# Kernel tuning notes

Hardware: AMD Instinct MI355X
Metric: run time of the kernel (lower is better)

## Reference

```python
import jax, jax.numpy as jnp
import numpy as np

N_NODES = 100000
N_EDGES = 3200000
IN_DIM = 512
HIDDEN = 16
N_CLASSES = 7


def setup_inputs() -> dict:
    key = jax.random.key(0)
    k1, k2, k3, k4 = jax.random.split(key, 4)
    x = jax.random.normal(k1, (N_NODES, IN_DIM), dtype=jnp.float32)
    edge_index = jax.random.randint(k2, (2, N_EDGES), 0, N_NODES, dtype=jnp.int32)
    W1 = jax.random.normal(k3, (IN_DIM, HIDDEN), dtype=jnp.float32) / np.sqrt(IN_DIM)
    b1 = jnp.zeros((HIDDEN,), dtype=jnp.float32)
    W2 = jax.random.normal(k4, (HIDDEN, N_CLASSES), dtype=jnp.float32) / np.sqrt(HIDDEN)
    b2 = jnp.zeros((N_CLASSES,), dtype=jnp.float32)
    return {"x": x, "edge_index": edge_index, "W1": W1, "b1": b1, "W2": W2, "b2": b2}


def _gcn_norm(edge_index, num_nodes):
    # Add self loops and compute symmetric normalization D^{-1/2} A D^{-1/2}
    loop = jnp.arange(num_nodes, dtype=edge_index.dtype)
    src = jnp.concatenate([edge_index[0], loop])
    dst = jnp.concatenate([edge_index[1], loop])
    deg = jax.ops.segment_sum(jnp.ones_like(dst, dtype=jnp.float32), dst,
                              num_segments=num_nodes)
    dinv = jnp.where(deg > 0, jax.lax.rsqrt(deg), 0.0)
    norm = dinv[src] * dinv[dst]  # [E + N]
    return src, dst, norm


def _gcn_conv(x, W, b, src, dst, norm, num_nodes):
    h = x @ W                                   # [N, out] dense GEMM first (PyG order)
    msg = h[src] * norm[:, None]                # gather + per-edge scale
    agg = jax.ops.segment_sum(msg, dst, num_segments=num_nodes)  # scatter-add
    return agg + b


def reference(x, edge_index, W1, b1, W2, b2):
    n = x.shape[0]
    src, dst, norm = _gcn_norm(edge_index, n)
    h = _gcn_conv(x, W1, b1, src, dst, norm, n)
    h = jax.nn.relu(h)
    # dropout is identity in eval mode (deterministic reference)
    out = _gcn_conv(h, W2, b2, src, dst, norm, n)
    return jax.nn.log_softmax(out, axis=1)
```

## Files before the change

### kernel.cpp

```cpp
#include <hip/hip_runtime.h>

#define N_NODES 100000
#define N_EDGES 3200000
#define IN_DIM  512
#define HIDDEN  16
#define NCLS    7

#define BSH     9
#define BNODES  512
#define NB      ((N_NODES + BNODES - 1) / BNODES)

#define EPB1    8192
#define NBLK1   ((N_EDGES + EPB1 - 1) / EPB1)
#define EPB2    4096
#define NBLK2   ((N_EDGES + EPB2 - 1) / EPB2)

__global__ void k_zero(int* __restrict__ bcnt, int* __restrict__ rowstart) {
    int i = threadIdx.x;
    bcnt[i] = 0;
    if (i == 0) rowstart[N_NODES] = N_EDGES;
}

__global__ __launch_bounds__(256) void k_bcount(const int* __restrict__ dst,
                                                int* __restrict__ bcnt) {
    __shared__ int hist[256];
    int tid = threadIdx.x;
    hist[tid] = 0;
    __syncthreads();
    int e0 = blockIdx.x * EPB1;
    int n  = min(EPB1, N_EDGES - e0);
    for (int k = tid; k < n; k += 256)
        atomicAdd(&hist[dst[e0 + k] >> BSH], 1);
    __syncthreads();
    int c = hist[tid];
    if (c) atomicAdd(&bcnt[tid], c);
}

__global__ __launch_bounds__(256) void k_bscan(const int* __restrict__ bcnt,
                                               int* __restrict__ bstart,
                                               int* __restrict__ bcur) {
    __shared__ int s[256];
    int tid = threadIdx.x;
    int c = bcnt[tid];
    s[tid] = c;
    __syncthreads();
    for (int off = 1; off < 256; off <<= 1) {
        int t = (tid >= off) ? s[tid - off] : 0;
        __syncthreads();
        s[tid] += t;
        __syncthreads();
    }
    if (tid == 0) bstart[0] = 0;
    bstart[tid + 1] = s[tid];
    bcur[tid]       = s[tid] - c;
}

__global__ __launch_bounds__(256) void k_bscatter(const int* __restrict__ src,
                                                  const int* __restrict__ dst,
                                                  int* __restrict__ bcur,
                                                  unsigned int* __restrict__ ebuf) {
    __shared__ unsigned int pk[EPB2];
    __shared__ unsigned char bb[EPB2];
    __shared__ int hist[256], base[256], lcur[256];
    int tid = threadIdx.x;
    hist[tid] = 0; lcur[tid] = 0;
    __syncthreads();
    int e0 = blockIdx.x * EPB2;
    int n  = min(EPB2, N_EDGES - e0);
    for (int k = tid; k < n; k += 256) {
        int d = dst[e0 + k];
        int b = d >> BSH;
        pk[k] = ((unsigned int)src[e0 + k] << BSH) | (unsigned int)(d & (BNODES - 1));
        bb[k] = (unsigned char)b;
        atomicAdd(&hist[b], 1);
    }
    __syncthreads();
    int h = hist[tid];
    base[tid] = h ? atomicAdd(&bcur[tid], h) : 0;
    __syncthreads();
    for (int k = tid; k < n; k += 256) {
        int b = bb[k];
        int pos = atomicAdd(&lcur[b], 1);
        ebuf[base[b] + pos] = pk[k];
    }
}

__global__ __launch_bounds__(512) void k_bsort(const int* __restrict__ bstart,
                                               const unsigned int* __restrict__ ebuf,
                                               int* __restrict__ rowstart,
                                               float* __restrict__ dinv,
                                               int* __restrict__ csr_src) {
    __shared__ int hist[512], cur[512];
    int tid = threadIdx.x;
    int b   = blockIdx.x;
    int e0 = bstart[b], e1 = bstart[b + 1];
    hist[tid] = 0;
    __syncthreads();
    for (int i = e0 + tid; i < e1; i += 512)
        atomicAdd(&hist[ebuf[i] & (BNODES - 1)], 1);
    __syncthreads();
    int deg = hist[tid];
    for (int off = 1; off < 512; off <<= 1) {
        int t = (tid >= off) ? hist[tid - off] : 0;
        __syncthreads();
        hist[tid] += t;
        __syncthreads();
    }
    int excl = hist[tid] - deg;
    int node = (b << BSH) + tid;
    if (node < N_NODES) {
        rowstart[node] = e0 + excl;
        dinv[node]     = rsqrtf((float)(deg + 1));
    }
    cur[tid] = excl;
    __syncthreads();
    for (int i = e0 + tid; i < e1; i += 512) {
        unsigned int p = ebuf[i];
        int pos = atomicAdd(&cur[p & (BNODES - 1)], 1);
        csr_src[e0 + pos] = (int)(p >> BSH);
    }
}

__global__ __launch_bounds__(256) void k_gemm1(
    const float* __restrict__ x, const float* __restrict__ W1,
    const float* __restrict__ dinv, float* __restrict__ h1s) {
    __shared__ float Xs[256 * 33];
    const int tid = threadIdx.x;
    const int n0  = blockIdx.x * 256;
    const int n   = n0 + tid;

    float acc[16];
#pragma unroll
    for (int j = 0; j < 16; ++j) acc[j] = 0.f;

    for (int kc = 0; kc < IN_DIM; kc += 32) {
        __syncthreads();
#pragma unroll
        for (int r = 0; r < 8; ++r) {
            int flat = r * 256 + tid;
            int row  = flat >> 3;
            int col  = (flat & 7) << 2;
            int gn   = n0 + row;
            if (gn < N_NODES) {
                const float4 v = *(const float4*)(x + (size_t)gn * IN_DIM + kc + col);
                float* d = &Xs[row * 33 + col];
                d[0] = v.x; d[1] = v.y; d[2] = v.z; d[3] = v.w;
            }
        }
        __syncthreads();
        if (n < N_NODES) {
#pragma unroll
            for (int i = 0; i < 32; ++i) {
                float xv = Xs[tid * 33 + i];
                const float* wr = W1 + (size_t)(kc + i) * 16;
#pragma unroll
                for (int j = 0; j < 16; ++j) acc[j] = fmaf(xv, wr[j], acc[j]);
            }
        }
    }

    if (n < N_NODES) {
        float di = dinv[n];
#pragma unroll
        for (int j = 0; j < 16; j += 4) {
            *(float4*)(h1s + (size_t)n * 16 + j) =
                make_float4(acc[j] * di, acc[j+1] * di, acc[j+2] * di, acc[j+3] * di);
        }
    }
}

__global__ __launch_bounds__(256) void k_agg1(
    const int* __restrict__ rowstart, const int* __restrict__ csr_src,
    const float* __restrict__ h1s, const float* __restrict__ dinv,
    const float* __restrict__ b1, float* __restrict__ z) {
    int gid = blockIdx.x * 256 + threadIdx.x;
    int g = gid >> 4, j = gid & 15;
    bool valid = g < N_NODES;
    int n = valid ? g : (N_NODES - 1);
    int start = rowstart[n], end = rowstart[n + 1];
    float acc = h1s[(size_t)n * 16 + j];
#pragma unroll 4
    for (int i = start; i < end; ++i) {
        int s = csr_src[i];
        acc += h1s[(size_t)s * 16 + j];
    }
    if (valid) {
        float v = dinv[n] * acc + b1[j];
        z[(size_t)n * 16 + j] = fmaxf(v, 0.f);
    }
}

__global__ __launch_bounds__(256) void k_layer2(
    const float* __restrict__ z, const float* __restrict__ W2,
    const float* __restrict__ dinv, float* __restrict__ h2s) {
    int n = blockIdx.x * 256 + threadIdx.x;
    if (n >= N_NODES) return;
    float zv[16];
#pragma unroll
    for (int k = 0; k < 16; k += 4) {
        float4 v = *(const float4*)(z + (size_t)n * 16 + k);
        zv[k] = v.x; zv[k+1] = v.y; zv[k+2] = v.z; zv[k+3] = v.w;
    }
    float di = dinv[n];
    float o[8];
#pragma unroll
    for (int jj = 0; jj < 7; ++jj) {
        float a = 0.f;
#pragma unroll
        for (int k = 0; k < 16; ++k) a = fmaf(zv[k], W2[k * 7 + jj], a);
        o[jj] = a * di;
    }
    o[7] = 0.f;
    *(float4*)(h2s + (size_t)n * 8 + 0) = make_float4(o[0], o[1], o[2], o[3]);
    *(float4*)(h2s + (size_t)n * 8 + 4) = make_float4(o[4], o[5], o[6], o[7]);
}

__global__ __launch_bounds__(256) void k_agg2(
    const int* __restrict__ rowstart, const int* __restrict__ csr_src,
    const float* __restrict__ h2s, const float* __restrict__ dinv,
    const float* __restrict__ b2, float* __restrict__ out) {
    int gid = blockIdx.x * 256 + threadIdx.x;
    int g = gid >> 3, j = gid & 7;
    bool valid = g < N_NODES;
    int n = valid ? g : (N_NODES - 1);
    int start = rowstart[n], end = rowstart[n + 1];
    float acc = h2s[(size_t)n * 8 + j];
#pragma unroll 4
    for (int i = start; i < end; ++i) {
        int s = csr_src[i];
        acc += h2s[(size_t)s * 8 + j];
    }
    float v = dinv[n] * acc + ((j < 7) ? b2[j] : -1e30f);
    float m = v;
    m = fmaxf(m, __shfl_xor(m, 1));
    m = fmaxf(m, __shfl_xor(m, 2));
    m = fmaxf(m, __shfl_xor(m, 4));
    float e = (j < 7) ? expf(v - m) : 0.f;
    float ssum = e;
    ssum += __shfl_xor(ssum, 1);
    ssum += __shfl_xor(ssum, 2);
    ssum += __shfl_xor(ssum, 4);
    float ls = logf(ssum) + m;
    if (valid && j < 7) out[(size_t)n * 7 + j] = v - ls;
}

extern "C" void kernel_launch(void* const* d_in, const int* in_sizes, int n_in,
                              void* d_out, int out_size, void* d_ws, size_t ws_size,
                              hipStream_t stream) {
    const float* x  = (const float*)d_in[0];
    const int*   ei = (const int*)d_in[1];
    const float* W1 = (const float*)d_in[2];
    const float* b1 = (const float*)d_in[3];
    const float* W2 = (const float*)d_in[4];
    const float* b2 = (const float*)d_in[5];
    float* out = (float*)d_out;

    const int* src = ei;
    const int* dst = ei + N_EDGES;

    char* ws = (char*)d_ws;
    size_t o = 0;
    auto alloc = [&](size_t bytes) -> void* {
        void* p = ws + o;
        o = (o + bytes + 255) & ~(size_t)255;
        return p;
    };
    int*   bcnt     = (int*)alloc(256 * 4);
    int*   bstart   = (int*)alloc(257 * 4);
    int*   bcur     = (int*)alloc(256 * 4);
    int*   rowstart = (int*)alloc(((size_t)N_NODES + 1) * 4);
    float* dinv     = (float*)alloc((size_t)N_NODES * 4);
    int*   csr_src  = (int*)alloc((size_t)N_EDGES * 4);
    char*  uni      = (char*)alloc((size_t)N_EDGES * 4);
    unsigned int* ebuf = (unsigned int*)uni;
    float* h1s      = (float*)uni;
    float* z        = h1s + (size_t)N_NODES * 16;
    float* h2s      = (float*)alloc((size_t)N_NODES * 8 * 4);

    const int nb_n = (N_NODES + 255) / 256;

    k_zero    <<<1, 256, 0, stream>>>(bcnt, rowstart);
    k_bcount  <<<NBLK1, 256, 0, stream>>>(dst, bcnt);
    k_bscan   <<<1, 256, 0, stream>>>(bcnt, bstart, bcur);
    k_bscatter<<<NBLK2, 256, 0, stream>>>(src, dst, bcur, ebuf);
    k_bsort   <<<NB, 512, 0, stream>>>(bstart, ebuf, rowstart, dinv, csr_src);
    k_gemm1   <<<nb_n, 256, 0, stream>>>(x, W1, dinv, h1s);
    k_agg1    <<<(N_NODES * 16 + 255) / 256, 256, 0, stream>>>(rowstart, csr_src, h1s, dinv, b1, z);
    k_layer2  <<<nb_n, 256, 0, stream>>>(z, W2, dinv, h2s);
    k_agg2    <<<(N_NODES * 8 + 255) / 256, 256, 0, stream>>>(rowstart, csr_src, h2s, dinv, b2, out);
}
```

Baseline: 515.7 us.

## Rewrite first-layer GEMM as persistent wave-per-row with register-resident weights

Replaces the shared-memory tiled x@W1 kernel with a persistent grid where each 64-lane wavefront handles one node row at a time. Each lane keeps its 8x16 slice of W1 in registers, reads x with coalesced float4 loads while prefetching the next row, and combines the 16 outputs using a butterfly of xor shuffles. This removes the LDS staging, the block syncs and the repeated per-thread W1 reads, so the kernel is meant to stream x at full memory bandwidth. The cost is high register pressure (128 weight floats per lane) and many shuffles per row.

```diff
diff --git a/kernel.cpp b/kernel.cpp
--- a/kernel.cpp
+++ b/kernel.cpp
@@ -14,6 +14,8 @@
 #define NBLK1   ((N_EDGES + EPB1 - 1) / EPB1)
 #define EPB2    4096
 #define NBLK2   ((N_EDGES + EPB2 - 1) / EPB2)
+
+#define GEMM1_BLOCKS 512
 
 __global__ void k_zero(int* __restrict__ bcnt, int* __restrict__ rowstart) {
     int i = threadIdx.x;
@@ -121,51 +123,86 @@
     }
 }
 
-__global__ __launch_bounds__(256) void k_gemm1(
+__global__ __launch_bounds__(256, 2) void k_gemm1(
     const float* __restrict__ x, const float* __restrict__ W1,
     const float* __restrict__ dinv, float* __restrict__ h1s) {
-    __shared__ float Xs[256 * 33];
     const int tid = threadIdx.x;
-    const int n0  = blockIdx.x * 256;
-    const int n   = n0 + tid;
-
-    float acc[16];
-#pragma unroll
-    for (int j = 0; j < 16; ++j) acc[j] = 0.f;
-
-    for (int kc = 0; kc < IN_DIM; kc += 32) {
-        __syncthreads();
-#pragma unroll
-        for (int r = 0; r < 8; ++r) {
-            int flat = r * 256 + tid;
-            int row  = flat >> 3;
-            int col  = (flat & 7) << 2;
-            int gn   = n0 + row;
-            if (gn < N_NODES) {
-                const float4 v = *(const float4*)(x + (size_t)gn * IN_DIM + kc + col);
-                float* d = &Xs[row * 33 + col];
-                d[0] = v.x; d[1] = v.y; d[2] = v.z; d[3] = v.w;
-            }
-        }
-        __syncthreads();
-        if (n < N_NODES) {
-#pragma unroll
-            for (int i = 0; i < 32; ++i) {
-                float xv = Xs[tid * 33 + i];
-                const float* wr = W1 + (size_t)(kc + i) * 16;
-#pragma unroll
-                for (int j = 0; j < 16; ++j) acc[j] = fmaf(xv, wr[j], acc[j]);
-            }
-        }
-    }
-
-    if (n < N_NODES) {
+    const int l   = tid & 63;
+    const int wid = blockIdx.x * 4 + (tid >> 6);
+    const int nw  = GEMM1_BLOCKS * 4;
+
+    float w[8][16];
+#pragma unroll
+    for (int q = 0; q < 4; ++q) {
+#pragma unroll
+        for (int c = 0; c < 4; ++c) {
+            float4 t0 = *(const float4*)(W1 + (size_t)(4 * l + q) * 16 + 4 * c);
+            w[q][4*c+0] = t0.x; w[q][4*c+1] = t0.y; w[q][4*c+2] = t0.z; w[q][4*c+3] = t0.w;
+            float4 t1 = *(const float4*)(W1 + (size_t)(256 + 4 * l + q) * 16 + 4 * c);
+            w[4+q][4*c+0] = t1.x; w[4+q][4*c+1] = t1.y; w[4+q][4*c+2] = t1.z; w[4+q][4*c+3] = t1.w;
+        }
+    }
+
+    const int b0 = l & 1, b1 = (l >> 1) & 1, b2 = (l >> 2) & 1, b3 = (l >> 3) & 1;
+
+    int n = wid;
+    if (n >= N_NODES) return;
+    const float* xr = x + (size_t)n * IN_DIM;
+    float4 v0 = *(const float4*)(xr + 4 * l);
+    float4 v1 = *(const float4*)(xr + 256 + 4 * l);
+
+    for (;;) {
+        int n2 = n + nw;
+        int np = (n2 < N_NODES) ? n2 : n;
+        const float* xp = x + (size_t)np * IN_DIM;
+        float4 u0 = *(const float4*)(xp + 4 * l);
+        float4 u1 = *(const float4*)(xp + 256 + 4 * l);
+
+        float p[16];
+#pragma unroll
+        for (int j = 0; j < 16; ++j) {
+            float a = v0.x * w[0][j];
+            a = fmaf(v0.y, w[1][j], a);
+            a = fmaf(v0.z, w[2][j], a);
+            a = fmaf(v0.w, w[3][j], a);
+            a = fmaf(v1.x, w[4][j], a);
+            a = fmaf(v1.y, w[5][j], a);
+            a = fmaf(v1.z, w[6][j], a);
+            a = fmaf(v1.w, w[7][j], a);
+            p[j] = a;
+        }
+
+        float q8[8];
+#pragma unroll
+        for (int m = 0; m < 8; ++m) {
+            float keep = b0 ? p[2*m+1] : p[2*m];
+            float give = b0 ? p[2*m]   : p[2*m+1];
+            q8[m] = keep + __shfl_xor(give, 1);
+        }
+        float r4[4];
+#pragma unroll
+        for (int t = 0; t < 4; ++t) {
+            float keep = b1 ? q8[2*t+1] : q8[2*t];
+            float give = b1 ? q8[2*t]   : q8[2*t+1];
+            r4[t] = keep + __shfl_xor(give, 2);
+        }
+        float s2[2];
+#pragma unroll
+        for (int u = 0; u < 2; ++u) {
+            float keep = b2 ? r4[2*u+1] : r4[2*u];
+            float give = b2 ? r4[2*u]   : r4[2*u+1];
+            s2[u] = keep + __shfl_xor(give, 4);
+        }
+        float t0 = (b3 ? s2[1] : s2[0]) + __shfl_xor(b3 ? s2[0] : s2[1], 8);
+        t0 += __shfl_xor(t0, 16);
+        t0 += __shfl_xor(t0, 32);
+
         float di = dinv[n];
-#pragma unroll
-        for (int j = 0; j < 16; j += 4) {
-            *(float4*)(h1s + (size_t)n * 16 + j) =
-                make_float4(acc[j] * di, acc[j+1] * di, acc[j+2] * di, acc[j+3] * di);
-        }
+        if (l < 16) h1s[(size_t)n * 16 + l] = t0 * di;
+
+        n = n2;
+        if (n >= N_NODES) break;
+        v0 = u0; v1 = u1;
     }
 }
 
@@ -284,7 +321,7 @@
     k_bscan   <<<1, 256, 0, stream>>>(bcnt, bstart, bcur);
     k_bscatter<<<NBLK2, 256, 0, stream>>>(src, dst, bcur, ebuf);
     k_bsort   <<<NB, 512, 0, stream>>>(bstart, ebuf, rowstart, dinv, csr_src);
-    k_gemm1   <<<nb_n, 256, 0, stream>>>(x, W1, dinv, h1s);
+    k_gemm1   <<<GEMM1_BLOCKS, 256, 0, stream>>>(x, W1, dinv, h1s);
     k_agg1    <<<(N_NODES * 16 + 255) / 256, 256, 0, stream>>>(rowstart, csr_src, h1s, dinv, b1, z);
     k_layer2  <<<nb_n, 256, 0, stream>>>(z, W2, dinv, h2s);
     k_agg2    <<<(N_NODES * 8 + 255) / 256, 256, 0, stream>>>(rowstart, csr_src, h2s, dinv, b2, out);
```

Result: faster. 462.7 us (-10.3%).
